# Performance work log

Measured on AMD Instinct MI355X. Metric: run time of the kernel, lower is better.

The kernel has to match this reference:

```python
import jax, jax.numpy as jnp
import numpy as np
import math

B, H, W, D = 4, 64, 64, 256
N, K, V = 8, 32, 32


def setup_inputs() -> dict:
    key = jax.random.key(0)
    ks = jax.random.split(key, 7)
    blob = jax.random.normal(ks[0], (B, H, W, D), dtype=jnp.float32)
    # 1x1 conv kernels == dense [D, out] matrices; glorot-ish scale
    s = 1.0 / math.sqrt(D)
    wq = jax.random.normal(ks[1], (D, N * K), dtype=jnp.float32) * s
    wk = jax.random.normal(ks[2], (D, N * K), dtype=jnp.float32) * s
    wv = jax.random.normal(ks[3], (D, N * V), dtype=jnp.float32) * s
    bq = jnp.zeros((N * K,), jnp.float32)
    bk = jnp.zeros((N * K,), jnp.float32)
    bv = jnp.zeros((N * V,), jnp.float32)
    return {"blob": blob, "wq": wq, "bq": bq, "wk": wk, "bk": bk, "wv": wv, "bv": bv}


def _maxpool2x2(x):
    # MaxPool2D with pool_size=strides=(2,2), VALID padding, NHWC
    return jax.lax.reduce_window(
        x, -jnp.inf, jax.lax.max,
        window_dimensions=(1, 2, 2, 1), window_strides=(1, 2, 2, 1), padding="VALID")


def reference(blob, wq, bq, wk, bk, wv, bv):
    H2, W2 = H // 2, W // 2
    # pooled query path
    q = _maxpool2x2(blob)                                   # [B,H2,W2,D]
    q = (q @ wq + bq).reshape(B, H2, W2, N, K)              # [B,H2,W2,N,K]
    q = q * (1.0 / math.sqrt(float(K)))
    # key/value paths (1x1 conv == per-pixel matmul); swish on value
    k = (blob @ wk + bk).reshape(B, H * W, N, K)            # [B,HW,N,K]
    v = jax.nn.swish(blob @ wv + bv).reshape(B, H * W, N, V)  # [B,HW,N,V]
    # cross-attention: contract K, outer product of pooled grid with full grid
    scores = jnp.einsum("bhwnk,bink->bhwin", q, k)          # [B,H2,W2,HW,N]
    attn = jax.nn.softmax(scores, axis=3)                   # softmax over HW
    out = jnp.einsum("bhwin,binv->bhwnv", attn, v)          # [B,H2,W2,N,V]
    return out.reshape(B, H2, W2, N * V)
```

## Files before the change

kernel.cpp:

```cpp
#include <hip/hip_runtime.h>


typedef _Float16 f16x8 __attribute__((ext_vector_type(8)));
typedef _Float16 f16x4 __attribute__((ext_vector_type(4)));
typedef float    f32x4 __attribute__((ext_vector_type(4)));

#define F16(x) static_cast<_Float16>(x)

#if __has_builtin(__builtin_amdgcn_exp2f)
#define EXP2(x) __builtin_amdgcn_exp2f(x)
#else
#define EXP2(x) exp2f(x)
#endif

__device__ __forceinline__ void gl_lds16(const void* g, void* l) {
    __builtin_amdgcn_global_load_lds(
        (const __attribute__((address_space(1))) unsigned int*)g,
        (__attribute__((address_space(3))) unsigned int*)l, 16, 0, 0);
}

__global__ __launch_bounds__(256) void prep_kernel(
    const float* __restrict__ wq, const float* __restrict__ wk,
    const float* __restrict__ wv, _Float16* __restrict__ wt) {
    __shared__ float t[32][33];
    const int blk = blockIdx.x;
    const int mat = blk >> 6;
    const int tile = blk & 63;
    const int d0 = (tile >> 3) * 32, o0 = (tile & 7) * 32;
    const float* w = (mat == 0) ? wq : (mat == 1 ? wk : wv);
    const int tx = threadIdx.x & 31, ty = threadIdx.x >> 5;
#pragma unroll
    for (int i = 0; i < 4; ++i)
        t[ty + i * 8][tx] = w[(d0 + ty + i * 8) * 256 + o0 + tx];
    __syncthreads();
#pragma unroll
    for (int i = 0; i < 4; ++i)
        wt[(mat << 16) + (o0 + ty + i * 8) * 256 + d0 + tx] = (_Float16)t[tx][ty + i * 8];
}

__global__ __launch_bounds__(256) void proj_kernel(
    const float* __restrict__ blob, const _Float16* __restrict__ wt,
    const float* __restrict__ bq, const float* __restrict__ bk, const float* __restrict__ bv,
    _Float16* __restrict__ qo, _Float16* __restrict__ ko, _Float16* __restrict__ vo) {
    __shared__ __align__(16) char atile[2][4096];

    const int tid = threadIdx.x;
    const int lane = tid & 63, wid = tid >> 6;
    const int quad = lane >> 4, l16 = lane & 15;
    int jb = blockIdx.x;
    int job, rowblk;
    if (jb < 64)       { job = 0; rowblk = jb; }
    else if (jb < 320) { job = 1; rowblk = jb - 64; }
    else               { job = 2; rowblk = jb - 320; }
    const int rowbase = rowblk * 64;
    const int colbase = wid * 64;
    const _Float16* wmat = wt + ((size_t)job << 16);
    const float* bias = (job == 0) ? bq : (job == 1 ? bk : bv);

    const int srow = tid >> 2, sc8 = tid & 3;
    const int sslot = srow * 4 + ((sc8 + (srow >> 2)) & 3);
    const float* aptr;
    if (job == 0) {
        const int grow = rowbase + srow;
        const int bb = grow >> 10, y = (grow >> 5) & 31, x = grow & 31;
        aptr = blob + (((bb * 64 + 2 * y) * 64) + 2 * x) * 256 + sc8 * 8;
    } else {
        aptr = blob + (size_t)(rowbase + srow) * 256 + sc8 * 8;
    }

    const _Float16* wptr[4];
#pragma unroll
    for (int nt = 0; nt < 4; ++nt)
        wptr[nt] = wmat + (size_t)(colbase + nt * 16 + l16) * 256 + quad * 8;

    const int aread = l16 * 64 + ((quad + (l16 >> 2)) & 3) * 16;

    f32x4 acc[4][4];
#pragma unroll
    for (int mc = 0; mc < 4; ++mc)
#pragma unroll
        for (int nt = 0; nt < 4; ++nt) acc[mc][nt] = (f32x4){0.f, 0.f, 0.f, 0.f};

    f16x8 wf[2][4];
    float4 ar[2][2];

    auto A_LOAD = [&](int t, float4* dst) {
        const float* p = aptr + t * 32;
        if (job == 0) {
            float4 a0 = *(const float4*)(p);
            float4 a1 = *(const float4*)(p + 4);
            float4 b0 = *(const float4*)(p + 256);
            float4 b1 = *(const float4*)(p + 260);
            float4 c0 = *(const float4*)(p + 16384);
            float4 c1 = *(const float4*)(p + 16388);
            float4 d0 = *(const float4*)(p + 16640);
            float4 d1 = *(const float4*)(p + 16644);
            dst[0].x = fmaxf(fmaxf(a0.x, b0.x), fmaxf(c0.x, d0.x));
            dst[0].y = fmaxf(fmaxf(a0.y, b0.y), fmaxf(c0.y, d0.y));
            dst[0].z = fmaxf(fmaxf(a0.z, b0.z), fmaxf(c0.z, d0.z));
            dst[0].w = fmaxf(fmaxf(a0.w, b0.w), fmaxf(c0.w, d0.w));
            dst[1].x = fmaxf(fmaxf(a1.x, b1.x), fmaxf(c1.x, d1.x));
            dst[1].y = fmaxf(fmaxf(a1.y, b1.y), fmaxf(c1.y, d1.y));
            dst[1].z = fmaxf(fmaxf(a1.z, b1.z), fmaxf(c1.z, d1.z));
            dst[1].w = fmaxf(fmaxf(a1.w, b1.w), fmaxf(c1.w, d1.w));
        } else {
            dst[0] = *(const float4*)(p);
            dst[1] = *(const float4*)(p + 4);
        }
    };
    auto A_WRITE = [&](int buf, const float4* src) {
        auto c0 = __builtin_amdgcn_cvt_pkrtz(src[0].x, src[0].y);
        auto c1 = __builtin_amdgcn_cvt_pkrtz(src[0].z, src[0].w);
        auto c2 = __builtin_amdgcn_cvt_pkrtz(src[1].x, src[1].y);
        auto c3 = __builtin_amdgcn_cvt_pkrtz(src[1].z, src[1].w);
        f16x8 v = {F16(c0[0]), F16(c0[1]), F16(c1[0]), F16(c1[1]),
                   F16(c2[0]), F16(c2[1]), F16(c3[0]), F16(c3[1])};
        *(f16x8*)(atile[buf] + sslot * 16) = v;
    };
    auto W_LOAD = [&](int t, f16x8* dst) {
#pragma unroll
        for (int nt = 0; nt < 4; ++nt) dst[nt] = *(const f16x8*)(wptr[nt] + t * 32);
    };

    W_LOAD(0, wf[0]);
    A_LOAD(0, ar[0]);
    A_WRITE(0, ar[0]);
    A_LOAD(1, ar[1]);
    asm volatile("s_waitcnt lgkmcnt(0)\n\ts_barrier" ::: "memory");

#pragma unroll
    for (int s = 0; s < 8; ++s) {
        if (s < 7) W_LOAD(s + 1, wf[(s + 1) & 1]);
        f16x8 af[4];
#pragma unroll
        for (int mc = 0; mc < 4; ++mc)
            af[mc] = *(const f16x8*)(atile[s & 1] + mc * 1024 + aread);
#pragma unroll
        for (int mc = 0; mc < 4; ++mc)
#pragma unroll
            for (int nt = 0; nt < 4; ++nt)
                acc[mc][nt] = __builtin_amdgcn_mfma_f32_16x16x32_f16(
                    af[mc], wf[s & 1][nt], acc[mc][nt], 0, 0, 0);
        if (s < 7) A_WRITE((s + 1) & 1, ar[(s + 1) & 1]);
        if (s < 6) A_LOAD(s + 2, ar[s & 1]);
        if (s < 7) asm volatile("s_waitcnt lgkmcnt(0)\n\ts_barrier" ::: "memory");
    }

#pragma unroll
    for (int nt = 0; nt < 4; ++nt) {
        const int o = colbase + nt * 16 + l16;
        const float bs = bias[o];
        const int nh = o >> 5, kk = o & 31;
#pragma unroll
        for (int mc = 0; mc < 4; ++mc) {
            if (job == 0) {
#pragma unroll
                for (int r = 0; r < 4; ++r) {
                    const int grow = rowbase + mc * 16 + quad * 4 + r;
                    const float x = (acc[mc][nt][r] + bs) * 0.25503508f;
                    const int bb = grow >> 10, mm = grow & 1023;
                    qo[(((bb * 8 + nh) * 1024 + mm) << 5) + kk] = (_Float16)x;
                }
            } else if (job == 1) {
#pragma unroll
                for (int r = 0; r < 4; ++r) {
                    const int grow = rowbase + mc * 16 + quad * 4 + r;
                    const float x = acc[mc][nt][r] + bs;
                    const int bb = grow >> 12, ii = grow & 4095;
                    ko[(((bb * 8 + nh) * 4096 + ii) << 5) + kk] = (_Float16)x;
                }
            } else {
                const int grow0 = rowbase + mc * 16 + quad * 4;
                const int bb = grow0 >> 12, i0 = grow0 & 4095;
                f16x4 pv;
#pragma unroll
                for (int r = 0; r < 4; ++r) {
                    float x = acc[mc][nt][r] + bs;
                    const float sg = 1.0f / (1.0f + __expf(-x));
                    pv[r] = (_Float16)(x * sg);
                }
                *(f16x4*)(vo + (size_t)(bb * 8 + nh) * 131072 + (i0 >> 4) * 512
                             + ((kk & 15) + quad * 16) * 8 + (kk >> 4) * 4) = pv;
            }
        }
    }
}

__global__ __launch_bounds__(512, 4) void attn_kernel(
    const _Float16* __restrict__ qb,
    const _Float16* __restrict__ kb,
    const _Float16* __restrict__ vf,
    float* __restrict__ out) {
    __shared__ __align__(16) char pool[49152];

    const int tid = threadIdx.x;
    const int lane = tid & 63, wid = tid >> 6;
    const int quad = lane >> 4, l16 = lane & 15;
    const int bn = blockIdx.x & 31, mt = blockIdx.x >> 5;
    const int b = bn >> 3, n = bn & 7;
    const int m0 = mt * 64;
    const int rg = wid & 3, kc = wid >> 2;

    const _Float16* gsrc[2];
    int ldsoff[2];
#pragma unroll
    for (int jj = 0; jj < 2; ++jj) {
        const int j = wid + jj * 8;
        const int kcj = j >> 3, sub = j & 7;
        if (sub < 4) {
            gsrc[jj] = kb + ((size_t)bn << 17)
                     + (size_t)(kcj * 2048 + sub * 16 + (lane & 15)) * 32 + (lane >> 4) * 8;
            ldsoff[jj] = kcj * 24576 + sub * 1024;
        } else {
            gsrc[jj] = vf + ((size_t)bn << 17)
                     + (size_t)(kcj * 128 + (sub - 4)) * 512 + lane * 8;
            ldsoff[jj] = kcj * 24576 + 4096 + (sub - 4) * 1024;
        }
    }

    const f16x8 qf = *(const f16x8*)(qb + (((size_t)(bn << 10) + m0 + rg * 16 + l16) << 5) + quad * 8);

    const int rbase = kc * 24576 + lane * 16;

#pragma unroll
    for (int p = 0; p < 2; ++p)
#pragma unroll
        for (int jj = 0; jj < 2; ++jj) {
            gl_lds16(gsrc[jj], pool + ldsoff[jj] + p * 8192);
            gsrc[jj] += 2048;
        }
    asm volatile("s_waitcnt vmcnt(2)\n\ts_barrier" ::: "memory");

    f32x4 acc0 = (f32x4){0.f, 0.f, 0.f, 0.f};
    f32x4 acc1 = acc0;
    float ps0 = 0.f;

    for (int s = 0; s < 32; ++s) {
        if (s < 30) {
            const int nb = ((s + 2) % 3) * 8192;
#pragma unroll
            for (int jj = 0; jj < 2; ++jj) {
                gl_lds16(gsrc[jj], pool + ldsoff[jj] + nb);
                gsrc[jj] += 2048;
            }
        }
        const char* base = pool + rbase + (s % 3) * 8192;
#pragma unroll
        for (int tloc = 0; tloc < 4; ++tloc) {
            const f16x8 kf = *(const f16x8*)(base + tloc * 1024);
            const f16x8 vv = *(const f16x8*)(base + 4096 + tloc * 1024);
            const f16x4 va0 = {vv[0], vv[1], vv[2], vv[3]};
            const f16x4 va1 = {vv[4], vv[5], vv[6], vv[7]};

            f32x4 s0 = __builtin_amdgcn_mfma_f32_16x16x32_f16(kf, qf, (f32x4){0.f,0.f,0.f,0.f}, 0, 0, 0);
            const float p0 = EXP2(s0[0]), p1 = EXP2(s0[1]), p2 = EXP2(s0[2]), p3 = EXP2(s0[3]);
            ps0 += (p0 + p1) + (p2 + p3);
            auto e0 = __builtin_amdgcn_cvt_pkrtz(p0, p1);
            auto e1 = __builtin_amdgcn_cvt_pkrtz(p2, p3);
            const f16x4 pb = {F16(e0[0]), F16(e0[1]), F16(e1[0]), F16(e1[1])};
            acc0 = __builtin_amdgcn_mfma_f32_16x16x16f16(va0, pb, acc0, 0, 0, 0);
            acc1 = __builtin_amdgcn_mfma_f32_16x16x16f16(va1, pb, acc1, 0, 0, 0);
        }
        if (s < 30)       asm volatile("s_waitcnt vmcnt(2)\n\ts_barrier" ::: "memory");
        else if (s == 30) asm volatile("s_waitcnt vmcnt(0)\n\ts_barrier" ::: "memory");
        else              asm volatile("s_barrier" ::: "memory");
    }

    float* num = (float*)pool;
    float* den = (float*)(pool + 64 * 33 * 4);
    for (int i = tid; i < 64 * 33 + 64; i += 512) ((float*)pool)[i] = 0.f;
    __syncthreads();

    ps0 += __shfl_xor(ps0, 16); ps0 += __shfl_xor(ps0, 32);

    const int m = rg * 16 + l16;
#pragma unroll
    for (int r = 0; r < 4; ++r) {
        atomicAdd(&num[m * 33 + quad * 4 + r], acc0[r]);
        atomicAdd(&num[m * 33 + 16 + quad * 4 + r], acc1[r]);
    }
    if (quad == 0) atomicAdd(&den[m], ps0);
    __syncthreads();

    {
        const int mloc = tid >> 3, v4 = (tid & 7) * 4;
        const float inv = 1.0f / den[mloc];
        const float* nr = num + mloc * 33 + v4;
        float4 o = {nr[0] * inv, nr[1] * inv, nr[2] * inv, nr[3] * inv};
        *(float4*)(out + (((size_t)(b << 10) + m0 + mloc) << 8) + n * 32 + v4) = o;
    }
}

extern "C" void kernel_launch(void* const* d_in, const int* in_sizes, int n_in,
                              void* d_out, int out_size, void* d_ws, size_t ws_size,
                              hipStream_t stream) {
    const float* blob = (const float*)d_in[0];
    const float* wq = (const float*)d_in[1];
    const float* bq = (const float*)d_in[2];
    const float* wk = (const float*)d_in[3];
    const float* bk = (const float*)d_in[4];
    const float* wv = (const float*)d_in[5];
    const float* bv = (const float*)d_in[6];
    float* out = (float*)d_out;

    char* ws = (char*)d_ws;
    _Float16* wt = (_Float16*)(ws);
    _Float16* ko = (_Float16*)(ws + 393216);
    _Float16* vo = (_Float16*)(ws + 8781824);
    _Float16* qo = (_Float16*)(ws + 17170432);

    prep_kernel<<<192, 256, 0, stream>>>(wq, wk, wv, wt);
    proj_kernel<<<576, 256, 0, stream>>>(blob, wt, bq, bk, bv, qo, ko, vo);
    attn_kernel<<<512, 512, 0, stream>>>(qo, ko, vo, out);
}
```

Before: 133.8 us.

## Split attention key range across two blocks with global atomic reduction

The attention kernel now splits the 4096-key sequence into two halves handled by separate blocks, doubling the grid from 512 to 1024 blocks. Each block atomically adds its partial numerator and denominator into zeroed global buffers, and the last block to arrive (tracked by a ticket counter) normalises and writes the output. The prep kernel zeroes these buffers, and launch bounds are raised to target more waves per SIMD. This aims to improve occupancy and CU fill, at the cost of global atomics, extra memory traffic and a threadfence handshake.

```diff
diff --git a/kernel.cpp b/kernel.cpp
--- a/kernel.cpp
+++ b/kernel.cpp
@@ -21,7 +21,8 @@
 
 __global__ __launch_bounds__(256) void prep_kernel(
     const float* __restrict__ wq, const float* __restrict__ wk,
-    const float* __restrict__ wv, _Float16* __restrict__ wt) {
+    const float* __restrict__ wv, _Float16* __restrict__ wt,
+    float4* __restrict__ gz) {
     __shared__ float t[32][33];
     const int blk = blockIdx.x;
     const int mat = blk >> 6;
@@ -29,6 +30,10 @@
     const int d0 = (tile >> 3) * 32, o0 = (tile & 7) * 32;
     const float* w = (mat == 0) ? wq : (mat == 1 ? wk : wv);
     const int tx = threadIdx.x & 31, ty = threadIdx.x >> 5;
+
+    const float4 z4 = {0.f, 0.f, 0.f, 0.f};
+    for (int i = blk * 256 + threadIdx.x; i < 270464; i += 192 * 256) gz[i] = z4;
+
 #pragma unroll
     for (int i = 0; i < 4; ++i)
         t[ty + i * 8][tx] = w[(d0 + ty + i * 8) * 256 + o0 + tx];
@@ -186,17 +191,22 @@
     }
 }
 
-__global__ __launch_bounds__(512, 4) void attn_kernel(
+__global__ __launch_bounds__(512, 6) void attn_kernel(
     const _Float16* __restrict__ qb,
     const _Float16* __restrict__ kb,
     const _Float16* __restrict__ vf,
-    float* __restrict__ out) {
+    float* __restrict__ out,
+    float* __restrict__ gnum,
+    float* __restrict__ gden,
+    int*   __restrict__ gtick) {
     __shared__ __align__(16) char pool[49152];
 
     const int tid = threadIdx.x;
     const int lane = tid & 63, wid = tid >> 6;
     const int quad = lane >> 4, l16 = lane & 15;
-    const int bn = blockIdx.x & 31, mt = blockIdx.x >> 5;
+    const int bn = blockIdx.x & 31;
+    const int mt = (blockIdx.x >> 5) & 15;
+    const int ks = blockIdx.x >> 9;
     const int b = bn >> 3, n = bn & 7;
     const int m0 = mt * 64;
     const int rg = wid & 3, kc = wid >> 2;
@@ -209,11 +219,12 @@
         const int kcj = j >> 3, sub = j & 7;
         if (sub < 4) {
             gsrc[jj] = kb + ((size_t)bn << 17)
-                     + (size_t)(kcj * 2048 + sub * 16 + (lane & 15)) * 32 + (lane >> 4) * 8;
+                     + (size_t)(ks * 2048 + kcj * 1024 + sub * 16 + (lane & 15)) * 32
+                     + (lane >> 4) * 8;
             ldsoff[jj] = kcj * 24576 + sub * 1024;
         } else {
             gsrc[jj] = vf + ((size_t)bn << 17)
-                     + (size_t)(kcj * 128 + (sub - 4)) * 512 + lane * 8;
+                     + (size_t)(ks * 128 + kcj * 64 + (sub - 4)) * 512 + lane * 8;
             ldsoff[jj] = kcj * 24576 + 4096 + (sub - 4) * 1024;
         }
     }
@@ -235,8 +246,8 @@
     f32x4 acc1 = acc0;
     float ps0 = 0.f;
 
-    for (int s = 0; s < 32; ++s) {
-        if (s < 30) {
+    for (int s = 0; s < 16; ++s) {
+        if (s < 14) {
             const int nb = ((s + 2) % 3) * 8192;
 #pragma unroll
             for (int jj = 0; jj < 2; ++jj) {
@@ -261,13 +272,14 @@
             acc0 = __builtin_amdgcn_mfma_f32_16x16x16f16(va0, pb, acc0, 0, 0, 0);
             acc1 = __builtin_amdgcn_mfma_f32_16x16x16f16(va1, pb, acc1, 0, 0, 0);
         }
-        if (s < 30)       asm volatile("s_waitcnt vmcnt(2)\n\ts_barrier" ::: "memory");
-        else if (s == 30) asm volatile("s_waitcnt vmcnt(0)\n\ts_barrier" ::: "memory");
+        if (s < 14)       asm volatile("s_waitcnt vmcnt(2)\n\ts_barrier" ::: "memory");
+        else if (s == 14) asm volatile("s_waitcnt vmcnt(0)\n\ts_barrier" ::: "memory");
         else              asm volatile("s_barrier" ::: "memory");
     }
 
     float* num = (float*)pool;
     float* den = (float*)(pool + 64 * 33 * 4);
+    int*  fin  = (int*)(pool + 64 * 33 * 4 + 256);
     for (int i = tid; i < 64 * 33 + 64; i += 512) ((float*)pool)[i] = 0.f;
     __syncthreads();
 
@@ -282,11 +294,30 @@
     if (quad == 0) atomicAdd(&den[m], ps0);
     __syncthreads();
 
+    const int gbase = bn * 16 + mt;
+    float* gn = gnum + (size_t)gbase * 2048;
+    float* gd = gden + gbase * 64;
+    const int mloc = tid >> 3, v4 = (tid & 7) * 4;
     {
-        const int mloc = tid >> 3, v4 = (tid & 7) * 4;
-        const float inv = 1.0f / den[mloc];
         const float* nr = num + mloc * 33 + v4;
-        float4 o = {nr[0] * inv, nr[1] * inv, nr[2] * inv, nr[3] * inv};
+        atomicAdd(&gn[mloc * 32 + v4 + 0], nr[0]);
+        atomicAdd(&gn[mloc * 32 + v4 + 1], nr[1]);
+        atomicAdd(&gn[mloc * 32 + v4 + 2], nr[2]);
+        atomicAdd(&gn[mloc * 32 + v4 + 3], nr[3]);
+        if (tid < 64) atomicAdd(&gd[tid], den[tid]);
+    }
+    __threadfence();
+    if (tid == 0) *fin = (atomicAdd(&gtick[gbase], 1) == 1);
+    __syncthreads();
+    if (!*fin) return;
+
+    __threadfence();
+    {
+        volatile const float* vgn = gn;
+        volatile const float* vgd = gd;
+        const float inv = 1.0f / vgd[mloc];
+        float4 o = {vgn[mloc * 32 + v4 + 0] * inv, vgn[mloc * 32 + v4 + 1] * inv,
+                    vgn[mloc * 32 + v4 + 2] * inv, vgn[mloc * 32 + v4 + 3] * inv};
         *(float4*)(out + (((size_t)(b << 10) + m0 + mloc) << 8) + n * 32 + v4) = o;
     }
 }
@@ -308,8 +339,11 @@
     _Float16* ko = (_Float16*)(ws + 393216);
     _Float16* vo = (_Float16*)(ws + 8781824);
     _Float16* qo = (_Float16*)(ws + 17170432);
-
-    prep_kernel<<<192, 256, 0, stream>>>(wq, wk, wv, wt);
+    float*  gnum = (float*)(ws + 19267584);
+    float*  gden = (float*)(ws + 23461888);
+    int*   gtick = (int*)(ws + 23592960);
+
+    prep_kernel<<<192, 256, 0, stream>>>(wq, wk, wv, wt, (float4*)(ws + 19267584));
     proj_kernel<<<576, 256, 0, stream>>>(blob, wt, bq, bk, bv, qo, ko, vo);
-    attn_kernel<<<512, 512, 0, stream>>>(qo, ko, vo, out);
-}
+    attn_kernel<<<1024, 512, 0, stream>>>(qo, ko, vo, out, gnum, gden, gtick);
+}
```

Result: slower. 326.6 us (+144.0%).

## Repartition attention waves over key tiles so each K/V fragment serves four query groups

Applied to the files above, without the earlier changes.

Each wave previously owned one 16-row query group and walked four key tiles per stage, reading K and V fragments from LDS for every tile. Now each wave holds all four query groups in registers and handles one key tile per stage. Each K/V LDS read is reused across four score and PV MFMAs, which cuts LDS read traffic by a factor of four. In exchange it needs four times the accumulator and query registers, which may push past the budget for 4 blocks per SM. The final LDS atomic reduction also gets more contention, since every wave now adds into all 64 rows.

```diff
diff --git a/kernel.cpp b/kernel.cpp
--- a/kernel.cpp
+++ b/kernel.cpp
@@ -199,7 +199,7 @@
     const int bn = blockIdx.x & 31, mt = blockIdx.x >> 5;
     const int b = bn >> 3, n = bn & 7;
     const int m0 = mt * 64;
-    const int rg = wid & 3, kc = wid >> 2;
+    const int kc = wid & 1, ks = wid >> 1;
 
     const _Float16* gsrc[2];
     int ldsoff[2];
@@ -218,9 +218,13 @@
         }
     }
 
-    const f16x8 qf = *(const f16x8*)(qb + (((size_t)(bn << 10) + m0 + rg * 16 + l16) << 5) + quad * 8);
-
-    const int rbase = kc * 24576 + lane * 16;
+    f16x8 qf[4];
+#pragma unroll
+    for (int g = 0; g < 4; ++g)
+        qf[g] = *(const f16x8*)(qb + (((size_t)(bn << 10) + m0 + g * 16 + l16) << 5) + quad * 8);
+
+    const int kread = kc * 24576 + ks * 1024 + lane * 16;
+    const int vread = kread + 4096;
 
 #pragma unroll
     for (int p = 0; p < 2; ++p)
@@ -231,9 +235,13 @@
         }
     asm volatile("s_waitcnt vmcnt(2)\n\ts_barrier" ::: "memory");
 
-    f32x4 acc0 = (f32x4){0.f, 0.f, 0.f, 0.f};
-    f32x4 acc1 = acc0;
-    float ps0 = 0.f;
+    f32x4 acc[4][2];
+#pragma unroll
+    for (int g = 0; g < 4; ++g) {
+        acc[g][0] = (f32x4){0.f, 0.f, 0.f, 0.f};
+        acc[g][1] = acc[g][0];
+    }
+    float ps[4] = {0.f, 0.f, 0.f, 0.f};
 
     for (int s = 0; s < 32; ++s) {
         if (s < 30) {
@@ -244,22 +252,21 @@
                 gsrc[jj] += 2048;
             }
         }
-        const char* base = pool + rbase + (s % 3) * 8192;
-#pragma unroll
-        for (int tloc = 0; tloc < 4; ++tloc) {
-            const f16x8 kf = *(const f16x8*)(base + tloc * 1024);
-            const f16x8 vv = *(const f16x8*)(base + 4096 + tloc * 1024);
-            const f16x4 va0 = {vv[0], vv[1], vv[2], vv[3]};
-            const f16x4 va1 = {vv[4], vv[5], vv[6], vv[7]};
-
-            f32x4 s0 = __builtin_amdgcn_mfma_f32_16x16x32_f16(kf, qf, (f32x4){0.f,0.f,0.f,0.f}, 0, 0, 0);
+        const int bo = (s % 3) * 8192;
+        const f16x8 kf = *(const f16x8*)(pool + kread + bo);
+        const f16x8 vv = *(const f16x8*)(pool + vread + bo);
+        const f16x4 va0 = {vv[0], vv[1], vv[2], vv[3]};
+        const f16x4 va1 = {vv[4], vv[5], vv[6], vv[7]};
+#pragma unroll
+        for (int g = 0; g < 4; ++g) {
+            f32x4 s0 = __builtin_amdgcn_mfma_f32_16x16x32_f16(kf, qf[g], (f32x4){0.f,0.f,0.f,0.f}, 0, 0, 0);
             const float p0 = EXP2(s0[0]), p1 = EXP2(s0[1]), p2 = EXP2(s0[2]), p3 = EXP2(s0[3]);
-            ps0 += (p0 + p1) + (p2 + p3);
+            ps[g] += (p0 + p1) + (p2 + p3);
             auto e0 = __builtin_amdgcn_cvt_pkrtz(p0, p1);
             auto e1 = __builtin_amdgcn_cvt_pkrtz(p2, p3);
             const f16x4 pb = {F16(e0[0]), F16(e0[1]), F16(e1[0]), F16(e1[1])};
-            acc0 = __builtin_amdgcn_mfma_f32_16x16x16f16(va0, pb, acc0, 0, 0, 0);
-            acc1 = __builtin_amdgcn_mfma_f32_16x16x16f16(va1, pb, acc1, 0, 0, 0);
+            acc[g][0] = __builtin_amdgcn_mfma_f32_16x16x16f16(va0, pb, acc[g][0], 0, 0, 0);
+            acc[g][1] = __builtin_amdgcn_mfma_f32_16x16x16f16(va1, pb, acc[g][1], 0, 0, 0);
         }
         if (s < 30)       asm volatile("s_waitcnt vmcnt(2)\n\ts_barrier" ::: "memory");
         else if (s == 30) asm volatile("s_waitcnt vmcnt(0)\n\ts_barrier" ::: "memory");
@@ -271,15 +278,22 @@
     for (int i = tid; i < 64 * 33 + 64; i += 512) ((float*)pool)[i] = 0.f;
     __syncthreads();
 
-    ps0 += __shfl_xor(ps0, 16); ps0 += __shfl_xor(ps0, 32);
-
-    const int m = rg * 16 + l16;
-#pragma unroll
-    for (int r = 0; r < 4; ++r) {
-        atomicAdd(&num[m * 33 + quad * 4 + r], acc0[r]);
-        atomicAdd(&num[m * 33 + 16 + quad * 4 + r], acc1[r]);
-    }
-    if (quad == 0) atomicAdd(&den[m], ps0);
+#pragma unroll
+    for (int g = 0; g < 4; ++g) {
+        ps[g] += __shfl_xor(ps[g], 16);
+        ps[g] += __shfl_xor(ps[g], 32);
+    }
+
+#pragma unroll
+    for (int g = 0; g < 4; ++g) {
+        const int m = g * 16 + l16;
+#pragma unroll
+        for (int r = 0; r < 4; ++r) {
+            atomicAdd(&num[m * 33 + quad * 4 + r], acc[g][0][r]);
+            atomicAdd(&num[m * 33 + 16 + quad * 4 + r], acc[g][1][r]);
+        }
+        if (quad == 0) atomicAdd(&den[m], ps[g]);
+    }
     __syncthreads();
 
     {
```

Measured after the change: 164.8 us. +23.1%, slower.
